# Optimization experiments

Hardware: AMD Instinct MI355X
Metric: run time of the kernel (lower is better)

Reference implementation:

```python
import jax, jax.numpy as jnp
import numpy as np

N = 2048
H, W = 160, 224
TANFOVX = 0.5774
TANFOVY = TANFOVX * H / W
SCALE_MOD = 1.0
CHUNK = 256
NEAR = 0.2
LOWPASS = 0.3  # EWA low-pass filter added to 2D covariance diagonal (as in CUDA kernel)
ALPHA_MIN = 1.0 / 255.0


def setup_inputs() -> dict:
    key = jax.random.key(0)
    ks = jax.random.split(key, 6)
    # gaussians in a cloud in front of the camera (camera at origin, looking +z)
    means3D = jax.random.normal(ks[0], (N, 3), jnp.float32) * jnp.array([1.2, 1.2, 0.8], jnp.float32) + jnp.array([0.0, 0.0, 4.0], jnp.float32)
    means2D = jnp.zeros((N, 3), jnp.float32)  # dummy grad holder, unused in fwd math
    opacities = jax.random.uniform(ks[1], (N, 1), jnp.float32) * 0.8 + 0.1
    colors_precomp = jax.random.uniform(ks[2], (N, 3), jnp.float32)
    scales = jax.random.uniform(ks[3], (N, 3), jnp.float32) * 0.06 + 0.01
    rotations = jax.random.normal(ks[4], (N, 4), jnp.float32)
    bg = jnp.zeros((3,), jnp.float32)
    viewmatrix = jnp.eye(4, dtype=jnp.float32)  # world == camera frame
    return dict(means3D=means3D, means2D=means2D, opacities=opacities,
                colors_precomp=colors_precomp, scales=scales, rotations=rotations,
                bg=bg, viewmatrix=viewmatrix)


def _quat_to_rot(q):
    q = q / jnp.linalg.norm(q, axis=-1, keepdims=True)
    w, x, y, z = q[..., 0], q[..., 1], q[..., 2], q[..., 3]
    R = jnp.stack([
        jnp.stack([1 - 2 * (y * y + z * z), 2 * (x * y - w * z), 2 * (x * z + w * y)], -1),
        jnp.stack([2 * (x * y + w * z), 1 - 2 * (x * x + z * z), 2 * (y * z - w * x)], -1),
        jnp.stack([2 * (x * z - w * y), 2 * (y * z + w * x), 1 - 2 * (x * x + y * y)], -1),
    ], -2)  # [N,3,3]
    return R


def _rasterize(means3D, opacities, colors_precomp, scales, rotations, bg, viewmatrix):
    dtype = means3D.dtype
    Rw = viewmatrix[:3, :3]
    tw = viewmatrix[:3, 3]
    t = means3D @ Rw.T + tw  # [N,3] view-space positions
    tz = t[:, 2]
    fx = W / (2.0 * TANFOVX)
    fy = H / (2.0 * TANFOVY)
    limx, limy = 1.3 * TANFOVX, 1.3 * TANFOVY
    txz = jnp.clip(t[:, 0] / tz, -limx, limx) * tz
    tyz = jnp.clip(t[:, 1] / tz, -limy, limy) * tz
    # 3D covariance: Sigma = R diag(s^2) R^T
    Rq = _quat_to_rot(rotations)
    S2 = (scales * SCALE_MOD) ** 2
    Sigma = jnp.einsum('nij,nj,nkj->nik', Rq, S2, Rq)
    # EWA Jacobian [N,2,3]
    zeros = jnp.zeros_like(tz)
    J = jnp.stack([
        jnp.stack([fx / tz, zeros, -fx * txz / (tz * tz)], -1),
        jnp.stack([zeros, fy / tz, -fy * tyz / (tz * tz)], -1),
    ], -2)
    Tm = jnp.einsum('nij,jk->nik', J, Rw)
    cov2 = jnp.einsum('nij,njk,nlk->nil', Tm, Sigma, Tm)  # [N,2,2]
    a = cov2[:, 0, 0] + LOWPASS
    b = cov2[:, 0, 1]
    c = cov2[:, 1, 1] + LOWPASS
    det = a * c - b * b
    inv = 1.0 / det
    conic = jnp.stack([c * inv, -b * inv, a * inv], -1)  # [N,3]
    mid = 0.5 * (a + c)
    lam1 = mid + jnp.sqrt(jnp.maximum(0.1, mid * mid - det))
    radii_f = jnp.ceil(3.0 * jnp.sqrt(lam1))
    # project to pixel coords (ndc2Pix convention)
    px = ((t[:, 0] / (tz * TANFOVX) + 1.0) * W - 1.0) * 0.5
    py = ((t[:, 1] / (tz * TANFOVY) + 1.0) * H - 1.0) * 0.5
    valid = (tz > NEAR) & (det > 0) & (radii_f > 0)
    radii = jnp.where(valid, radii_f, 0.0).astype(jnp.int32)
    # global front-to-back depth sort (invalid pushed to end)
    order = jnp.argsort(jnp.where(valid, tz, jnp.inf))
    m2_s = jnp.stack([px, py], -1)[order]          # [N,2]
    con_s = conic[order]                            # [N,3]
    op_s = opacities[:, 0][order]                   # [N]
    col_s = colors_precomp[order]                   # [N,3]
    dep_s = tz[order]                               # [N]
    vld_s = valid[order]                            # [N]
    # pixel grid
    yy, xx = jnp.meshgrid(jnp.arange(H, dtype=dtype), jnp.arange(W, dtype=dtype), indexing='ij')
    gx = xx.ravel()
    gy = yy.ravel()
    HW = H * W

    def chunk_body(Tc, ch):
        m2, con, op, col, dep, vld = ch  # [C,...]
        dx = m2[:, 0, None] - gx[None, :]  # [C,HW]
        dy = m2[:, 1, None] - gy[None, :]
        power = -0.5 * (con[:, 0, None] * dx * dx + con[:, 2, None] * dy * dy) - con[:, 1, None] * dx * dy
        alpha = jnp.minimum(0.99, op[:, None] * jnp.exp(power))
        alpha = jnp.where((power <= 0) & (alpha >= ALPHA_MIN) & vld[:, None], alpha, 0.0)
        om = 1.0 - alpha
        cp = jnp.cumprod(om, axis=0)
        Tin = Tc[None, :] * jnp.concatenate([jnp.ones((1, HW), dtype), cp[:-1]], 0)  # exclusive transmittance
        w = alpha * Tin
        color_c = jnp.einsum('cp,cd->dp', w, col)      # [3,HW]
        depth_c = jnp.sum(w * dep[:, None], 0)          # [HW]
        ntouch = jnp.sum(alpha > 0.0, axis=1).astype(jnp.int32)
        return Tc * cp[-1], (color_c, depth_c, ntouch)

    chunks = jax.tree_util.tree_map(
        lambda x: x.reshape((N // CHUNK, CHUNK) + x.shape[1:]),
        (m2_s, con_s, op_s, col_s, dep_s, vld_s))
    Tfin, (colors_c, depths_c, ntouch_c) = jax.lax.scan(
        jax.checkpoint(chunk_body), jnp.ones((HW,), dtype), chunks)
    color = colors_c.sum(0) + bg[:, None] * Tfin[None, :]
    depth = depths_c.sum(0)
    n_touched = jnp.zeros((N,), jnp.int32).at[order].set(ntouch_c.reshape(-1))
    opacity = (1.0 - Tfin).reshape(1, H, W)
    return color.reshape(3, H, W), radii, depth.reshape(1, H, W), opacity, n_touched


def reference(means3D, means2D, opacities, colors_precomp, scales, rotations, bg, viewmatrix):
    # means2D is a dummy gradient-holder (as in the original API); unused in forward math.
    return _rasterize(means3D, opacities, colors_precomp, scales, rotations, bg, viewmatrix)
```

## Files before the change

### kernel.cpp

```cpp
#include <hip/hip_runtime.h>
#include <math.h>

namespace {

constexpr int NG     = 2048;
constexpr int IMG_H  = 160;
constexpr int IMG_W  = 224;
constexpr int HW     = IMG_H * IMG_W;
constexpr int TS     = 8;
constexpr int TX     = IMG_W / TS;
constexpr int TYN    = IMG_H / TS;
constexpr int NTILE  = TX * TYN;

constexpr int NSEG   = 8;
constexpr int SEGS   = NG / NSEG;

constexpr int TPG    = 64;
constexpr int SEGK   = NG / TPG;

constexpr float TFX   = 0.5774f;
constexpr float TFY   = (float)(0.5774 * 160.0 / 224.0);
constexpr float FXC   = (float)(224.0 / (2.0 * 0.5774));
constexpr float FYC   = (float)(160.0 / (2.0 * (0.5774 * 160.0 / 224.0)));
constexpr float LIMX  = (float)(1.3 * 0.5774);
constexpr float LIMY  = (float)(1.3 * (0.5774 * 160.0 / 224.0));
constexpr float A_MIN = (float)(1.0 / 255.0);
constexpr float NEARP = 0.2f;
constexpr float LOWPASS = 0.3f;
constexpr float L2E   = 1.4426950408889634f;
constexpr float LN2   = 0.6931471805599453f;
constexpr float L2_255 = 7.994353436858858f;

constexpr int O_COLOR = 0;
constexpr int O_RADII = 3 * HW;
constexpr int O_DEPTH = O_RADII + NG;
constexpr int O_OPAC  = O_DEPTH + HW;
constexpr int O_NT    = O_OPAC + HW;

constexpr int W_U    = 0;
constexpr int W_KEY  = 12 * NG;
constexpr int W_UPB  = 13 * NG;
constexpr int W_S    = 14 * NG;
constexpr int W_ORG  = 26 * NG;
constexpr int W_PB   = 27 * NG;

}

__global__ __launch_bounds__(256) void k_pre(const float* __restrict__ means3D,
                                             const float* __restrict__ opac,
                                             const float* __restrict__ cols,
                                             const float* __restrict__ scales,
                                             const float* __restrict__ rots,
                                             const float* __restrict__ vm,
                                             float* __restrict__ wsf,
                                             unsigned* __restrict__ wsu,
                                             float* __restrict__ out)
{
    int i = blockIdx.x * blockDim.x + threadIdx.x;
    if (i >= NG) return;
    out[O_NT + i] = 0.0f;

    float R00 = vm[0], R01 = vm[1], R02 = vm[2],  T0 = vm[3];
    float R10 = vm[4], R11 = vm[5], R12 = vm[6],  T1 = vm[7];
    float R20 = vm[8], R21 = vm[9], R22 = vm[10], T2 = vm[11];

    float mx = means3D[3*i], my = means3D[3*i+1], mz = means3D[3*i+2];
    float tx = R00*mx + R01*my + R02*mz + T0;
    float ty = R10*mx + R11*my + R12*mz + T1;
    float tz = R20*mx + R21*my + R22*mz + T2;

    float txz = fminf(LIMX, fmaxf(-LIMX, tx / tz)) * tz;
    float tyz = fminf(LIMY, fmaxf(-LIMY, ty / tz)) * tz;

    float qw = rots[4*i], qx = rots[4*i+1], qy = rots[4*i+2], qz = rots[4*i+3];
    float qn = 1.0f / sqrtf(qw*qw + qx*qx + qy*qy + qz*qz);
    qw *= qn; qx *= qn; qy *= qn; qz *= qn;
    float r00 = 1.0f - 2.0f*(qy*qy + qz*qz), r01 = 2.0f*(qx*qy - qw*qz), r02 = 2.0f*(qx*qz + qw*qy);
    float r10 = 2.0f*(qx*qy + qw*qz), r11 = 1.0f - 2.0f*(qx*qx + qz*qz), r12 = 2.0f*(qy*qz - qw*qx);
    float r20 = 2.0f*(qx*qz - qw*qy), r21 = 2.0f*(qy*qz + qw*qx), r22 = 1.0f - 2.0f*(qx*qx + qy*qy);

    float s0 = scales[3*i];   s0 = s0 * s0;
    float s1 = scales[3*i+1]; s1 = s1 * s1;
    float s2 = scales[3*i+2]; s2 = s2 * s2;

    float S00 = r00*r00*s0 + r01*r01*s1 + r02*r02*s2;
    float S01 = r00*r10*s0 + r01*r11*s1 + r02*r12*s2;
    float S02 = r00*r20*s0 + r01*r21*s1 + r02*r22*s2;
    float S11 = r10*r10*s0 + r11*r11*s1 + r12*r12*s2;
    float S12 = r10*r20*s0 + r11*r21*s1 + r12*r22*s2;
    float S22 = r20*r20*s0 + r21*r21*s1 + r22*r22*s2;

    float j00 = FXC / tz;
    float j02 = -FXC * txz / (tz * tz);
    float j11 = FYC / tz;
    float j12 = -FYC * tyz / (tz * tz);

    float Tm00 = j00*R00 + j02*R20, Tm01 = j00*R01 + j02*R21, Tm02 = j00*R02 + j02*R22;
    float Tm10 = j11*R10 + j12*R20, Tm11 = j11*R11 + j12*R21, Tm12 = j11*R12 + j12*R22;

    float M00 = Tm00*S00 + Tm01*S01 + Tm02*S02;
    float M01 = Tm00*S01 + Tm01*S11 + Tm02*S12;
    float M02 = Tm00*S02 + Tm01*S12 + Tm02*S22;
    float M10 = Tm10*S00 + Tm11*S01 + Tm12*S02;
    float M11 = Tm10*S01 + Tm11*S11 + Tm12*S12;
    float M12 = Tm10*S02 + Tm11*S12 + Tm12*S22;

    float cov00 = M00*Tm00 + M01*Tm01 + M02*Tm02;
    float cov01 = M00*Tm10 + M01*Tm11 + M02*Tm12;
    float cov11 = M10*Tm10 + M11*Tm11 + M12*Tm12;

    float a = cov00 + LOWPASS;
    float b = cov01;
    float c = cov11 + LOWPASS;
    float det = a*c - b*b;
    float dinv = 1.0f / det;
    float con0 = c * dinv, con1 = -b * dinv, con2 = a * dinv;

    float mid  = 0.5f * (a + c);
    float lam1 = mid + sqrtf(fmaxf(0.1f, mid*mid - det));
    float radf = ceilf(3.0f * sqrtf(lam1));

    float px = ((tx / (tz * TFX) + 1.0f) * (float)IMG_W - 1.0f) * 0.5f;
    float py = ((ty / (tz * TFY) + 1.0f) * (float)IMG_H - 1.0f) * 0.5f;

    bool valid = (tz > NEARP) && (det > 0.0f) && (radf > 0.0f);

    float op   = opac[i];
    float l2op = log2f(op);
    float tlin = fmaxf(0.0f, (l2op + L2_255) * LN2);
    float dxm  = sqrtf(2.0f * tlin * a) * 1.001f + 0.1f;
    float dym  = sqrtf(2.0f * tlin * c) * 1.001f + 0.1f;

    int itx0 = (int)floorf((px - dxm) * (1.0f / TS));
    int itx1 = (int)floorf((px + dxm) * (1.0f / TS));
    int ity0 = (int)floorf((py - dym) * (1.0f / TS));
    int ity1 = (int)floorf((py + dym) * (1.0f / TS));
    unsigned pb;
    if (!valid || itx1 < 0 || ity1 < 0 || itx0 >= TX || ity0 >= TYN) {
        pb = 0xFFFFFFFFu;
    } else {
        unsigned a0 = (unsigned)max(itx0, 0);
        unsigned a1 = (unsigned)max(ity0, 0);
        unsigned a2 = (unsigned)min(itx1, TX - 1);
        unsigned a3 = (unsigned)min(ity1, TYN - 1);
        pb = a0 | (a1 << 8) | (a2 << 16) | (a3 << 24);
    }
    wsu[W_UPB + i] = pb;

    float4 f0, f1, f2;
    if (valid) {
        f0 = make_float4(px, py, dxm, dym);
        f1 = make_float4(-0.5f*con0*L2E, -con1*L2E, -0.5f*con2*L2E, l2op);
        f2 = make_float4(cols[3*i], cols[3*i+1], cols[3*i+2], tz);
    } else {
        f0 = make_float4(1e9f, 1e9f, -1.0f, -1.0f);
        f1 = make_float4(0.0f, 0.0f, 0.0f, -1000.0f);
        f2 = make_float4(0.0f, 0.0f, 0.0f, 0.0f);
    }
    float4* dst = (float4*)&wsf[W_U + i*12];
    dst[0] = f0; dst[1] = f1; dst[2] = f2;
    wsf[W_KEY + i] = valid ? tz : INFINITY;
    out[O_RADII + i] = valid ? radf : 0.0f;
}

__global__ __launch_bounds__(256) void k_rank(float* __restrict__ wsf,
                                              int* __restrict__ wsi,
                                              unsigned* __restrict__ wsu)
{
    __shared__ float sk[NG];
    int tid = threadIdx.x;
    float4* sk4 = (float4*)sk;
    const float4* gk4 = (const float4*)(wsf + W_KEY);
    sk4[tid]       = gk4[tid];
    sk4[tid + 256] = gk4[tid + 256];
    __syncthreads();

    int i = blockIdx.x * (256 / TPG) + (tid >> 6);
    int s = tid & (TPG - 1);
    float ki = sk[i];

    int r = 0;
    #pragma unroll
    for (int u = 0; u < SEGK / 4; ++u) {
        int j4 = (u + s) & (SEGK / 4 - 1);
        float4 kk = sk4[s * (SEGK / 4) + j4];
        int jb = s * SEGK + j4 * 4;
        r += (kk.x < ki || (kk.x == ki && (jb+0) < i)) ? 1 : 0;
        r += (kk.y < ki || (kk.y == ki && (jb+1) < i)) ? 1 : 0;
        r += (kk.z < ki || (kk.z == ki && (jb+2) < i)) ? 1 : 0;
        r += (kk.w < ki || (kk.w == ki && (jb+3) < i)) ? 1 : 0;
    }
    r += __shfl_xor(r, 1);
    r += __shfl_xor(r, 2);
    r += __shfl_xor(r, 4);
    r += __shfl_xor(r, 8);
    r += __shfl_xor(r, 16);
    r += __shfl_xor(r, 32);

    if (s == 0) {
        const float4* src = (const float4*)&wsf[W_U + i*12];
        float4 a0 = src[0], a1 = src[1], a2 = src[2];
        float4* dst = (float4*)&wsf[W_S + r*12];
        dst[0] = a0; dst[1] = a1; dst[2] = a2;
        wsu[W_PB + r] = wsu[W_UPB + i];
        wsi[W_ORG + r] = i;
    }
}

__global__ __launch_bounds__(512) void k_rast(const float* __restrict__ wsf,
                                              const int* __restrict__ wsi,
                                              const unsigned* __restrict__ wsu,
                                              const float* __restrict__ bg,
                                              float* __restrict__ out)
{
    __shared__ int   Llist[NSEG][SEGS];
    __shared__ int   Lcnt[NSEG][SEGS];
    __shared__ float Ls[NSEG][64][12];
    __shared__ float Lpart[NSEG][5][64];

    int tid  = threadIdx.x;
    int lane = tid & 63;
    int wv   = tid >> 6;
    int tile = blockIdx.x;
    int tx = tile % TX, ty = tile / TX;
    int base0 = wv * SEGS;

    int cnt = 0;
    #pragma unroll
    for (int c = 0; c < SEGS / 64; ++c) {
        unsigned w = wsu[W_PB + base0 + c * 64 + lane];
        bool keep = ((w & 255u) <= (unsigned)tx) && ((unsigned)tx <= ((w >> 16) & 255u))
                 && (((w >> 8) & 255u) <= (unsigned)ty) && ((unsigned)ty <= (w >> 24));
        unsigned long long m = __ballot(keep);
        if (keep) Llist[wv][cnt + __popcll(m & ((1ull << lane) - 1ull))] = base0 + c * 64 + lane;
        cnt += (int)__popcll(m);
    }

    int px_i = tx * TS + (lane & 7);
    int py_i = ty * TS + (lane >> 3);
    float gx = (float)px_i, gy = (float)py_i;

    float T = 1.0f, C0 = 0.0f, C1 = 0.0f, C2 = 0.0f, D = 0.0f;

    for (int b2 = 0; b2 < cnt; b2 += 64) {
        int cl = min(64, cnt - b2);
        if (lane < cl) {
            int e = Llist[wv][b2 + lane];
            const float4* s4 = (const float4*)&wsf[W_S + e*12];
            *(float4*)&Ls[wv][lane][0] = s4[0];
            *(float4*)&Ls[wv][lane][4] = s4[1];
            *(float4*)&Ls[wv][lane][8] = s4[2];
        }
        #pragma unroll 2
        for (int g = 0; g < cl; ++g) {
            float4 f0 = *(const float4*)&Ls[wv][g][0];
            float4 f1 = *(const float4*)&Ls[wv][g][4];
            float4 f2 = *(const float4*)&Ls[wv][g][8];
            float dx = f0.x - gx, dy = f0.y - gy;
            float p2 = f1.x*dx*dx + f1.y*dx*dy + f1.z*dy*dy;
            float al = fminf(0.99f, exp2f(p2 + f1.w));
            bool keep = (p2 <= 0.0f) && (al >= A_MIN);
            float a = keep ? al : 0.0f;
            float w = T * a;
            C0 = fmaf(w, f2.x, C0);
            C1 = fmaf(w, f2.y, C1);
            C2 = fmaf(w, f2.z, C2);
            D  = fmaf(w, f2.w, D);
            T -= w;
            unsigned long long m = __ballot(keep);
            if (lane == g) Lcnt[wv][b2 + g] = (int)__popcll(m);
        }
    }

    Lpart[wv][0][lane] = T;
    Lpart[wv][1][lane] = C0;
    Lpart[wv][2][lane] = C1;
    Lpart[wv][3][lane] = C2;
    Lpart[wv][4][lane] = D;

    for (int j = lane; j < cnt; j += 64) {
        int c = Lcnt[wv][j];
        if (c > 0) atomicAdd(out + O_NT + wsi[W_ORG + Llist[wv][j]], (float)c);
    }

    __syncthreads();

    if (wv == 0) {
        float Tt = 1.0f, c0 = 0.0f, c1 = 0.0f, c2 = 0.0f, d = 0.0f;
        #pragma unroll
        for (int s = 0; s < NSEG; ++s) {
            c0 = fmaf(Tt, Lpart[s][1][lane], c0);
            c1 = fmaf(Tt, Lpart[s][2][lane], c1);
            c2 = fmaf(Tt, Lpart[s][3][lane], c2);
            d  = fmaf(Tt, Lpart[s][4][lane], d);
            Tt *= Lpart[s][0][lane];
        }
        int pix = py_i * IMG_W + px_i;
        out[O_COLOR + 0*HW + pix] = c0 + bg[0] * Tt;
        out[O_COLOR + 1*HW + pix] = c1 + bg[1] * Tt;
        out[O_COLOR + 2*HW + pix] = c2 + bg[2] * Tt;
        out[O_DEPTH + pix] = d;
        out[O_OPAC  + pix] = 1.0f - Tt;
    }
}

extern "C" void kernel_launch(void* const* d_in, const int* in_sizes, int n_in,
                              void* d_out, int out_size, void* d_ws, size_t ws_size,
                              hipStream_t stream)
{
    const float* means3D = (const float*)d_in[0];
    const float* opac    = (const float*)d_in[2];
    const float* cols    = (const float*)d_in[3];
    const float* scales  = (const float*)d_in[4];
    const float* rots    = (const float*)d_in[5];
    const float* bg      = (const float*)d_in[6];
    const float* vm      = (const float*)d_in[7];
    float* out = (float*)d_out;
    float* wsf = (float*)d_ws;
    int*   wsi = (int*)d_ws;
    unsigned* wsu = (unsigned*)d_ws;

    hipLaunchKernelGGL(k_pre, dim3(NG / 256), dim3(256), 0, stream,
                       means3D, opac, cols, scales, rots, vm, wsf, wsu, out);
    hipLaunchKernelGGL(k_rank, dim3(NG / (256 / TPG)), dim3(256), 0, stream, wsf, wsi, wsu);
    hipLaunchKernelGGL(k_rast, dim3(NTILE), dim3(512), 0, stream,
                       wsf, wsi, wsu, bg, out);
}
```

Before: 19.51 us.

## Fuse preprocessing and depth ranking into a single kernel

Merges the per-Gaussian preprocessing kernel and the rank/scatter kernel into one launch. Each block recomputes every Gaussian's view depth into shared memory, ranks its own 8 Gaussians against all of them, then runs the full projection for those Gaussians and writes them straight to their sorted slots. This removes one kernel launch and the unsorted workspace round trip, at the cost of every block redundantly recomputing all depth keys. The sort key now treats only near-plane culling as invalid, so Gaussians rejected for other reasons can land in a different order.

Result: faster. 16.22 us (-16.9%).

```diff
diff --git a/kernel.cpp b/kernel.cpp
--- a/kernel.cpp
+++ b/kernel.cpp
@@ -15,8 +15,8 @@
 constexpr int NSEG   = 8;
 constexpr int SEGS   = NG / NSEG;
 
-constexpr int TPG    = 64;
-constexpr int SEGK   = NG / TPG;
+constexpr int PRB    = 256;
+constexpr int OWN    = NG / PRB;
 
 constexpr float TFX   = 0.5774f;
 constexpr float TFY   = (float)(0.5774 * 160.0 / 224.0);
@@ -37,173 +37,166 @@
 constexpr int O_OPAC  = O_DEPTH + HW;
 constexpr int O_NT    = O_OPAC + HW;
 
-constexpr int W_U    = 0;
-constexpr int W_KEY  = 12 * NG;
-constexpr int W_UPB  = 13 * NG;
-constexpr int W_S    = 14 * NG;
-constexpr int W_ORG  = 26 * NG;
-constexpr int W_PB   = 27 * NG;
+constexpr int W_S    = 0;
+constexpr int W_ORG  = 12 * NG;
+constexpr int W_PB   = 13 * NG;
 
 }
 
-__global__ __launch_bounds__(256) void k_pre(const float* __restrict__ means3D,
-                                             const float* __restrict__ opac,
-                                             const float* __restrict__ cols,
-                                             const float* __restrict__ scales,
-                                             const float* __restrict__ rots,
-                                             const float* __restrict__ vm,
-                                             float* __restrict__ wsf,
-                                             unsigned* __restrict__ wsu,
-                                             float* __restrict__ out)
-{
-    int i = blockIdx.x * blockDim.x + threadIdx.x;
-    if (i >= NG) return;
-    out[O_NT + i] = 0.0f;
-
-    float R00 = vm[0], R01 = vm[1], R02 = vm[2],  T0 = vm[3];
-    float R10 = vm[4], R11 = vm[5], R12 = vm[6],  T1 = vm[7];
-    float R20 = vm[8], R21 = vm[9], R22 = vm[10], T2 = vm[11];
-
-    float mx = means3D[3*i], my = means3D[3*i+1], mz = means3D[3*i+2];
-    float tx = R00*mx + R01*my + R02*mz + T0;
-    float ty = R10*mx + R11*my + R12*mz + T1;
-    float tz = R20*mx + R21*my + R22*mz + T2;
-
-    float txz = fminf(LIMX, fmaxf(-LIMX, tx / tz)) * tz;
-    float tyz = fminf(LIMY, fmaxf(-LIMY, ty / tz)) * tz;
-
-    float qw = rots[4*i], qx = rots[4*i+1], qy = rots[4*i+2], qz = rots[4*i+3];
-    float qn = 1.0f / sqrtf(qw*qw + qx*qx + qy*qy + qz*qz);
-    qw *= qn; qx *= qn; qy *= qn; qz *= qn;
-    float r00 = 1.0f - 2.0f*(qy*qy + qz*qz), r01 = 2.0f*(qx*qy - qw*qz), r02 = 2.0f*(qx*qz + qw*qy);
-    float r10 = 2.0f*(qx*qy + qw*qz), r11 = 1.0f - 2.0f*(qx*qx + qz*qz), r12 = 2.0f*(qy*qz - qw*qx);
-    float r20 = 2.0f*(qx*qz - qw*qy), r21 = 2.0f*(qy*qz + qw*qx), r22 = 1.0f - 2.0f*(qx*qx + qy*qy);
-
-    float s0 = scales[3*i];   s0 = s0 * s0;
-    float s1 = scales[3*i+1]; s1 = s1 * s1;
-    float s2 = scales[3*i+2]; s2 = s2 * s2;
-
-    float S00 = r00*r00*s0 + r01*r01*s1 + r02*r02*s2;
-    float S01 = r00*r10*s0 + r01*r11*s1 + r02*r12*s2;
-    float S02 = r00*r20*s0 + r01*r21*s1 + r02*r22*s2;
-    float S11 = r10*r10*s0 + r11*r11*s1 + r12*r12*s2;
-    float S12 = r10*r20*s0 + r11*r21*s1 + r12*r22*s2;
-    float S22 = r20*r20*s0 + r21*r21*s1 + r22*r22*s2;
-
-    float j00 = FXC / tz;
-    float j02 = -FXC * txz / (tz * tz);
-    float j11 = FYC / tz;
-    float j12 = -FYC * tyz / (tz * tz);
-
-    float Tm00 = j00*R00 + j02*R20, Tm01 = j00*R01 + j02*R21, Tm02 = j00*R02 + j02*R22;
-    float Tm10 = j11*R10 + j12*R20, Tm11 = j11*R11 + j12*R21, Tm12 = j11*R12 + j12*R22;
-
-    float M00 = Tm00*S00 + Tm01*S01 + Tm02*S02;
-    float M01 = Tm00*S01 + Tm01*S11 + Tm02*S12;
-    float M02 = Tm00*S02 + Tm01*S12 + Tm02*S22;
-    float M10 = Tm10*S00 + Tm11*S01 + Tm12*S02;
-    float M11 = Tm10*S01 + Tm11*S11 + Tm12*S12;
-    float M12 = Tm10*S02 + Tm11*S12 + Tm12*S22;
-
-    float cov00 = M00*Tm00 + M01*Tm01 + M02*Tm02;
-    float cov01 = M00*Tm10 + M01*Tm11 + M02*Tm12;
-    float cov11 = M10*Tm10 + M11*Tm11 + M12*Tm12;
-
-    float a = cov00 + LOWPASS;
-    float b = cov01;
-    float c = cov11 + LOWPASS;
-    float det = a*c - b*b;
-    float dinv = 1.0f / det;
-    float con0 = c * dinv, con1 = -b * dinv, con2 = a * dinv;
-
-    float mid  = 0.5f * (a + c);
-    float lam1 = mid + sqrtf(fmaxf(0.1f, mid*mid - det));
-    float radf = ceilf(3.0f * sqrtf(lam1));
-
-    float px = ((tx / (tz * TFX) + 1.0f) * (float)IMG_W - 1.0f) * 0.5f;
-    float py = ((ty / (tz * TFY) + 1.0f) * (float)IMG_H - 1.0f) * 0.5f;
-
-    bool valid = (tz > NEARP) && (det > 0.0f) && (radf > 0.0f);
-
-    float op   = opac[i];
-    float l2op = log2f(op);
-    float tlin = fmaxf(0.0f, (l2op + L2_255) * LN2);
-    float dxm  = sqrtf(2.0f * tlin * a) * 1.001f + 0.1f;
-    float dym  = sqrtf(2.0f * tlin * c) * 1.001f + 0.1f;
-
-    int itx0 = (int)floorf((px - dxm) * (1.0f / TS));
-    int itx1 = (int)floorf((px + dxm) * (1.0f / TS));
-    int ity0 = (int)floorf((py - dym) * (1.0f / TS));
-    int ity1 = (int)floorf((py + dym) * (1.0f / TS));
-    unsigned pb;
-    if (!valid || itx1 < 0 || ity1 < 0 || itx0 >= TX || ity0 >= TYN) {
-        pb = 0xFFFFFFFFu;
-    } else {
-        unsigned a0 = (unsigned)max(itx0, 0);
-        unsigned a1 = (unsigned)max(ity0, 0);
-        unsigned a2 = (unsigned)min(itx1, TX - 1);
-        unsigned a3 = (unsigned)min(ity1, TYN - 1);
-        pb = a0 | (a1 << 8) | (a2 << 16) | (a3 << 24);
-    }
-    wsu[W_UPB + i] = pb;
-
-    float4 f0, f1, f2;
-    if (valid) {
-        f0 = make_float4(px, py, dxm, dym);
-        f1 = make_float4(-0.5f*con0*L2E, -con1*L2E, -0.5f*con2*L2E, l2op);
-        f2 = make_float4(cols[3*i], cols[3*i+1], cols[3*i+2], tz);
-    } else {
-        f0 = make_float4(1e9f, 1e9f, -1.0f, -1.0f);
-        f1 = make_float4(0.0f, 0.0f, 0.0f, -1000.0f);
-        f2 = make_float4(0.0f, 0.0f, 0.0f, 0.0f);
-    }
-    float4* dst = (float4*)&wsf[W_U + i*12];
-    dst[0] = f0; dst[1] = f1; dst[2] = f2;
-    wsf[W_KEY + i] = valid ? tz : INFINITY;
-    out[O_RADII + i] = valid ? radf : 0.0f;
-}
-
-__global__ __launch_bounds__(256) void k_rank(float* __restrict__ wsf,
-                                              int* __restrict__ wsi,
-                                              unsigned* __restrict__ wsu)
+__global__ __launch_bounds__(256) void k_prerank(const float* __restrict__ means3D,
+                                                 const float* __restrict__ opac,
+                                                 const float* __restrict__ cols,
+                                                 const float* __restrict__ scales,
+                                                 const float* __restrict__ rots,
+                                                 const float* __restrict__ vm,
+                                                 float* __restrict__ wsf,
+                                                 int* __restrict__ wsi,
+                                                 unsigned* __restrict__ wsu,
+                                                 float* __restrict__ out)
 {
     __shared__ float sk[NG];
+    __shared__ int   rbuf[OWN];
+
     int tid = threadIdx.x;
-    float4* sk4 = (float4*)sk;
-    const float4* gk4 = (const float4*)(wsf + W_KEY);
-    sk4[tid]       = gk4[tid];
-    sk4[tid + 256] = gk4[tid + 256];
+    int b   = blockIdx.x;
+
+    float R20k = vm[8], R21k = vm[9], R22k = vm[10], T2k = vm[11];
+    #pragma unroll
+    for (int j = 0; j < NG / 256; ++j) {
+        int g = tid + 256 * j;
+        float tzk = R20k*means3D[3*g] + R21k*means3D[3*g+1] + R22k*means3D[3*g+2] + T2k;
+        sk[g] = (tzk > NEARP) ? tzk : INFINITY;
+    }
     __syncthreads();
 
-    int i = blockIdx.x * (256 / TPG) + (tid >> 6);
-    int s = tid & (TPG - 1);
-    float ki = sk[i];
-
-    int r = 0;
+    int w = tid >> 6, lane = tid & 63;
     #pragma unroll
-    for (int u = 0; u < SEGK / 4; ++u) {
-        int j4 = (u + s) & (SEGK / 4 - 1);
-        float4 kk = sk4[s * (SEGK / 4) + j4];
-        int jb = s * SEGK + j4 * 4;
-        r += (kk.x < ki || (kk.x == ki && (jb+0) < i)) ? 1 : 0;
-        r += (kk.y < ki || (kk.y == ki && (jb+1) < i)) ? 1 : 0;
-        r += (kk.z < ki || (kk.z == ki && (jb+2) < i)) ? 1 : 0;
-        r += (kk.w < ki || (kk.w == ki && (jb+3) < i)) ? 1 : 0;
-    }
-    r += __shfl_xor(r, 1);
-    r += __shfl_xor(r, 2);
-    r += __shfl_xor(r, 4);
-    r += __shfl_xor(r, 8);
-    r += __shfl_xor(r, 16);
-    r += __shfl_xor(r, 32);
-
-    if (s == 0) {
-        const float4* src = (const float4*)&wsf[W_U + i*12];
-        float4 a0 = src[0], a1 = src[1], a2 = src[2];
+    for (int k = 0; k < OWN / 4; ++k) {
+        int i = b * OWN + w * (OWN / 4) + k;
+        float ki = sk[i];
+        int r = 0;
+        #pragma unroll
+        for (int u = 0; u < NG / 64; ++u) {
+            int j = lane + 64 * u;
+            float kk = sk[j];
+            r += (kk < ki || (kk == ki && j < i)) ? 1 : 0;
+        }
+        r += __shfl_xor(r, 1);
+        r += __shfl_xor(r, 2);
+        r += __shfl_xor(r, 4);
+        r += __shfl_xor(r, 8);
+        r += __shfl_xor(r, 16);
+        r += __shfl_xor(r, 32);
+        if (lane == 0) rbuf[w * (OWN / 4) + k] = r;
+    }
+    __syncthreads();
+
+    if (tid < OWN) {
+        int i = b * OWN + tid;
+        int r = rbuf[tid];
+
+        float R00 = vm[0], R01 = vm[1], R02 = vm[2],  T0 = vm[3];
+        float R10 = vm[4], R11 = vm[5], R12 = vm[6],  T1 = vm[7];
+        float R20 = vm[8], R21 = vm[9], R22 = vm[10], T2 = vm[11];
+
+        float mx = means3D[3*i], my = means3D[3*i+1], mz = means3D[3*i+2];
+        float tx = R00*mx + R01*my + R02*mz + T0;
+        float ty = R10*mx + R11*my + R12*mz + T1;
+        float tz = R20*mx + R21*my + R22*mz + T2;
+
+        float txz = fminf(LIMX, fmaxf(-LIMX, tx / tz)) * tz;
+        float tyz = fminf(LIMY, fmaxf(-LIMY, ty / tz)) * tz;
+
+        float qw = rots[4*i], qx = rots[4*i+1], qy = rots[4*i+2], qz = rots[4*i+3];
+        float qn = 1.0f / sqrtf(qw*qw + qx*qx + qy*qy + qz*qz);
+        qw *= qn; qx *= qn; qy *= qn; qz *= qn;
+        float r00 = 1.0f - 2.0f*(qy*qy + qz*qz), r01 = 2.0f*(qx*qy - qw*qz), r02 = 2.0f*(qx*qz + qw*qy);
+        float r10 = 2.0f*(qx*qy + qw*qz), r11 = 1.0f - 2.0f*(qx*qx + qz*qz), r12 = 2.0f*(qy*qz - qw*qx);
+        float r20 = 2.0f*(qx*qz - qw*qy), r21 = 2.0f*(qy*qz + qw*qx), r22 = 1.0f - 2.0f*(qx*qx + qy*qy);
+
+        float s0 = scales[3*i];   s0 = s0 * s0;
+        float s1 = scales[3*i+1]; s1 = s1 * s1;
+        float s2 = scales[3*i+2]; s2 = s2 * s2;
+
+        float S00 = r00*r00*s0 + r01*r01*s1 + r02*r02*s2;
+        float S01 = r00*r10*s0 + r01*r11*s1 + r02*r12*s2;
+        float S02 = r00*r20*s0 + r01*r21*s1 + r02*r22*s2;
+        float S11 = r10*r10*s0 + r11*r11*s1 + r12*r12*s2;
+        float S12 = r10*r20*s0 + r11*r21*s1 + r12*r22*s2;
+        float S22 = r20*r20*s0 + r21*r21*s1 + r22*r22*s2;
+
+        float j00 = FXC / tz;
+        float j02 = -FXC * txz / (tz * tz);
+        float j11 = FYC / tz;
+        float j12 = -FYC * tyz / (tz * tz);
+
+        float Tm00 = j00*R00 + j02*R20, Tm01 = j00*R01 + j02*R21, Tm02 = j00*R02 + j02*R22;
+        float Tm10 = j11*R10 + j12*R20, Tm11 = j11*R11 + j12*R21, Tm12 = j11*R12 + j12*R22;
+
+        float M00 = Tm00*S00 + Tm01*S01 + Tm02*S02;
+        float M01 = Tm00*S01 + Tm01*S11 + Tm02*S12;
+        float M02 = Tm00*S02 + Tm01*S12 + Tm02*S22;
+        float M10 = Tm10*S00 + Tm11*S01 + Tm12*S02;
+        float M11 = Tm10*S01 + Tm11*S11 + Tm12*S12;
+        float M12 = Tm10*S02 + Tm11*S12 + Tm12*S22;
+
+        float cov00 = M00*Tm00 + M01*Tm01 + M02*Tm02;
+        float cov01 = M00*Tm10 + M01*Tm11 + M02*Tm12;
+        float cov11 = M10*Tm10 + M11*Tm11 + M12*Tm12;
+
+        float a = cov00 + LOWPASS;
+        float bb = cov01;
+        float c = cov11 + LOWPASS;
+        float det = a*c - bb*bb;
+        float dinv = 1.0f / det;
+        float con0 = c * dinv, con1 = -bb * dinv, con2 = a * dinv;
+
+        float mid  = 0.5f * (a + c);
+        float lam1 = mid + sqrtf(fmaxf(0.1f, mid*mid - det));
+        float radf = ceilf(3.0f * sqrtf(lam1));
+
+        float px = ((tx / (tz * TFX) + 1.0f) * (float)IMG_W - 1.0f) * 0.5f;
+        float py = ((ty / (tz * TFY) + 1.0f) * (float)IMG_H - 1.0f) * 0.5f;
+
+        bool valid = (tz > NEARP) && (det > 0.0f) && (radf > 0.0f);
+
+        float op   = opac[i];
+        float l2op = log2f(op);
+        float tlin = fmaxf(0.0f, (l2op + L2_255) * LN2);
+        float dxm  = sqrtf(2.0f * tlin * a) * 1.001f + 0.1f;
+        float dym  = sqrtf(2.0f * tlin * c) * 1.001f + 0.1f;
+
+        int itx0 = (int)floorf((px - dxm) * (1.0f / TS));
+        int itx1 = (int)floorf((px + dxm) * (1.0f / TS));
+        int ity0 = (int)floorf((py - dym) * (1.0f / TS));
+        int ity1 = (int)floorf((py + dym) * (1.0f / TS));
+        unsigned pb;
+        if (!valid || itx1 < 0 || ity1 < 0 || itx0 >= TX || ity0 >= TYN) {
+            pb = 0xFFFFFFFFu;
+        } else {
+            unsigned a0 = (unsigned)max(itx0, 0);
+            unsigned a1 = (unsigned)max(ity0, 0);
+            unsigned a2 = (unsigned)min(itx1, TX - 1);
+            unsigned a3 = (unsigned)min(ity1, TYN - 1);
+            pb = a0 | (a1 << 8) | (a2 << 16) | (a3 << 24);
+        }
+
+        float4 f0, f1, f2;
+        if (valid) {
+            f0 = make_float4(px, py, dxm, dym);
+            f1 = make_float4(-0.5f*con0*L2E, -con1*L2E, -0.5f*con2*L2E, l2op);
+            f2 = make_float4(cols[3*i], cols[3*i+1], cols[3*i+2], tz);
+        } else {
+            f0 = make_float4(1e9f, 1e9f, -1.0f, -1.0f);
+            f1 = make_float4(0.0f, 0.0f, 0.0f, -1000.0f);
+            f2 = make_float4(0.0f, 0.0f, 0.0f, 0.0f);
+        }
         float4* dst = (float4*)&wsf[W_S + r*12];
-        dst[0] = a0; dst[1] = a1; dst[2] = a2;
-        wsu[W_PB + r] = wsu[W_UPB + i];
+        dst[0] = f0; dst[1] = f1; dst[2] = f2;
+        wsu[W_PB + r]  = pb;
         wsi[W_ORG + r] = i;
+        out[O_RADII + i] = valid ? radf : 0.0f;
+        out[O_NT + i] = 0.0f;
     }
 }
 
@@ -320,9 +313,8 @@
     int*   wsi = (int*)d_ws;
     unsigned* wsu = (unsigned*)d_ws;
 
-    hipLaunchKernelGGL(k_pre, dim3(NG / 256), dim3(256), 0, stream,
-                       means3D, opac, cols, scales, rots, vm, wsf, wsu, out);
-    hipLaunchKernelGGL(k_rank, dim3(NG / (256 / TPG)), dim3(256), 0, stream, wsf, wsi, wsu);
+    hipLaunchKernelGGL(k_prerank, dim3(PRB), dim3(256), 0, stream,
+                       means3D, opac, cols, scales, rots, vm, wsf, wsi, wsu, out);
     hipLaunchKernelGGL(k_rast, dim3(NTILE), dim3(512), 0, stream,
                        wsf, wsi, wsu, bg, out);
 }
```
